# Kernel tuning notes

Measured on AMD Instinct MI355X. Metric: run time of the kernel, lower is better.

The kernel has to match this reference:

```python
import jax, jax.numpy as jnp
import numpy as np

S, B, V, E, H, L = 500, 64, 50257, 512, 512, 2


def setup_inputs() -> dict:
    key = jax.random.key(0)
    ks = jax.random.split(key, 12)
    u = lambda k, shape, s: jax.random.uniform(k, shape, jnp.float32, -s, s)
    kstd = 1.0 / np.sqrt(H)
    return {
        "inputs": jax.random.randint(ks[0], (S, B), 0, V, dtype=jnp.int64),
        "text_lengths": jax.random.randint(ks[1], (B,), 1, S, dtype=jnp.int64),
        "embedding": jax.random.normal(ks[2], (V, E), jnp.float32),
        "W_ih": u(ks[3], (4 * H, E), kstd),   # PyTorch LSTM gate order: i,f,g,o
        "W_hh": u(ks[4], (4 * H, H), kstd),
        "b_ih": u(ks[5], (4 * H,), kstd),
        "b_hh": u(ks[6], (4 * H,), kstd),
        "W_word": u(ks[7], (H, H), 0.1),
        "b_word": jnp.zeros((H, 1), jnp.float32),
        "w_proj": u(ks[8], (H, 1), 0.1),
        "dec_W": u(ks[9], (L, H), kstd),
        "dec_b": u(ks[10], (L,), kstd),
    }


def _lstm(x, W_ih, W_hh, b_ih, b_hh):
    # x: [S, B, E] -> states [S, B, H]
    Bsz = x.shape[1]
    Hn = W_hh.shape[1]
    # precompute input projections for all timesteps in one GEMM
    xproj = jnp.einsum('sbe,ge->sbg', x, W_ih) + b_ih + b_hh  # [S, B, 4H]

    def step(carry, xp):
        h, c = carry
        z = xp + h @ W_hh.T  # [B, 4H]
        i, f, g, o = jnp.split(z, 4, axis=-1)
        i, f, o = jax.nn.sigmoid(i), jax.nn.sigmoid(f), jax.nn.sigmoid(o)
        c = f * c + i * jnp.tanh(g)
        h = o * jnp.tanh(c)
        return (h, c), h

    h0 = jnp.zeros((Bsz, Hn), x.dtype)
    _, hs = jax.lax.scan(step, (h0, h0), xproj)
    return hs  # [S, B, H]


def reference(inputs, text_lengths, embedding, W_ih, W_hh, b_ih, b_hh,
              W_word, b_word, w_proj, dec_W, dec_b):
    # eval mode: dropout is identity
    embedded = embedding[inputs]                       # [S, B, E]
    states = _lstm(embedded, W_ih, W_hh, b_ih, b_hh)   # [S, B, H]
    # batch_matmul_bias with tanh: tanh(states @ W_word + b_word^T)
    word_squish = jnp.tanh(jnp.einsum('sbh,hk->sbk', states, W_word) + b_word[:, 0])
    # batch_matmul: project to scalar score per (s, b)
    word_attn = jnp.einsum('sbh,hk->sbk', word_squish, w_proj)[..., 0]  # [S, B]
    # softmax over sequence dim (nn.Softmax on [B, S] -> dim=1)
    attn = jax.nn.softmax(word_attn.T, axis=1).T       # [S, B]
    # attention_mul: weighted sum over S, keepdim -> [1, B, H]
    pooled = jnp.einsum('sb,sbh->bh', attn, states)[None]
    return pooled @ dec_W.T + dec_b                    # [1, B, labels]
```

## Files before the change

### kernel.cpp

```cpp
#include <hip/hip_runtime.h>


#define S_LEN 500
#define BATCH 64
#define EDIM 512
#define HDIM 512
#define TEAMS 8
#define WGS_PER_TEAM 32
#define TB 8
#define NBLOCKS (TEAMS * WGS_PER_TEAM)
#define NTHREADS 512
#define NSLICE 8
#define SLICE_LEN 63

typedef unsigned long long ull;

#define XPROJ_BYTES  ((size_t)S_LEN * 2048 * BATCH * 4)
#define STATES_OFF   XPROJ_BYTES
#define STATES_BYTES ((size_t)S_LEN * BATCH * HDIM * 4)
#define HBUF_OFF     (STATES_OFF + STATES_BYTES)
#define HBUF_BYTES   ((size_t)2 * TEAMS * TB * HDIM * 8)
#define PART_OFF     (HBUF_OFF + HBUF_BYTES)
#define PART_BYTES   (4 * S_LEN * BATCH * 4)
#define POOLP_OFF    (PART_OFF + PART_BYTES)
#define POOLP_BYTES  ((size_t)BATCH * NSLICE * HDIM * 4)
#define ML_OFF       (POOLP_OFF + POOLP_BYTES)
#define ML_BYTES     (BATCH * NSLICE * 2 * 4)

__global__ __launch_bounds__(256) void xproj_gemm(
    const int* __restrict__ idx, const float* __restrict__ emb,
    const float* __restrict__ W_ih, const float* __restrict__ b_ih,
    const float* __restrict__ b_hh, float* __restrict__ xproj) {
  __shared__ float At[16][132];
  __shared__ float Bt[16][132];
  __shared__ int sidx[128];

  const int tid = threadIdx.x;
  const int sb0 = blockIdx.x * 128;
  const int g0  = blockIdx.y * 128;
  if (tid < 128) sidx[tid] = idx[sb0 + tid];

  const int ty = tid >> 4, tx = tid & 15;
  const int ra = tid & 127, pp = tid >> 7;

  float acc[8][8];
#pragma unroll
  for (int i = 0; i < 8; ++i)
#pragma unroll
    for (int j = 0; j < 8; ++j) acc[i][j] = 0.f;

  __syncthreads();

  for (int k0 = 0; k0 < 512; k0 += 16) {
    const float* pa = &W_ih[(size_t)(g0 + ra) * 512 + k0 + 8 * pp];
    float4 a0 = *(const float4*)pa, a1 = *(const float4*)(pa + 4);
    const float* pb = &emb[(size_t)sidx[ra] * 512 + k0 + 8 * pp];
    float4 b0 = *(const float4*)pb, b1 = *(const float4*)(pb + 4);
    At[8*pp+0][ra]=a0.x; At[8*pp+1][ra]=a0.y; At[8*pp+2][ra]=a0.z; At[8*pp+3][ra]=a0.w;
    At[8*pp+4][ra]=a1.x; At[8*pp+5][ra]=a1.y; At[8*pp+6][ra]=a1.z; At[8*pp+7][ra]=a1.w;
    Bt[8*pp+0][ra]=b0.x; Bt[8*pp+1][ra]=b0.y; Bt[8*pp+2][ra]=b0.z; Bt[8*pp+3][ra]=b0.w;
    Bt[8*pp+4][ra]=b1.x; Bt[8*pp+5][ra]=b1.y; Bt[8*pp+6][ra]=b1.z; Bt[8*pp+7][ra]=b1.w;
    __syncthreads();
#pragma unroll
    for (int kk = 0; kk < 16; ++kk) {
      float4 x0 = *(const float4*)&At[kk][ty * 8];
      float4 x1 = *(const float4*)&At[kk][ty * 8 + 4];
      float4 y0 = *(const float4*)&Bt[kk][tx * 8];
      float4 y1 = *(const float4*)&Bt[kk][tx * 8 + 4];
      float av[8] = {x0.x, x0.y, x0.z, x0.w, x1.x, x1.y, x1.z, x1.w};
      float bv[8] = {y0.x, y0.y, y0.z, y0.w, y1.x, y1.y, y1.z, y1.w};
#pragma unroll
      for (int i = 0; i < 8; ++i)
#pragma unroll
        for (int j = 0; j < 8; ++j) acc[i][j] = fmaf(av[i], bv[j], acc[i][j]);
    }
    __syncthreads();
  }
  const int sbb = sb0 + tx * 8;
  const int s  = sbb >> 6;
  const int tm = (sbb & 63) >> 3;
#pragma unroll
  for (int i = 0; i < 8; ++i) {
    const int g = g0 + ty * 8 + i;
    const float bias = b_ih[g] + b_hh[g];
    float* dst = &xproj[(((size_t)s * TEAMS + tm) * 2048 + g) * 8];
    float4 v0 = {acc[i][0] + bias, acc[i][1] + bias, acc[i][2] + bias, acc[i][3] + bias};
    float4 v1 = {acc[i][4] + bias, acc[i][5] + bias, acc[i][6] + bias, acc[i][7] + bias};
    *(float4*)dst = v0;
    *(float4*)(dst + 4) = v1;
  }
}

__global__ __launch_bounds__(NTHREADS, 1) void lstm_persistent(
    const float* __restrict__ xproj, const float* __restrict__ W_hh,
    float* __restrict__ states, ull* __restrict__ h_buf) {
  __shared__ float red[2][8][4][72];

  const int team = blockIdx.x & 7;
  const int wg   = blockIdx.x >> 3;
  const int tid  = threadIdx.x;
  const int wv   = tid >> 6;
  const int l    = tid & 63;

  const int g = 16 * wg + (l & 15) + 512 * (l >> 4);

  float whh[64];
  {
    const float4* phh = (const float4*)(W_hh + (size_t)g * HDIM + (size_t)wv * 64);
#pragma unroll
    for (int j = 0; j < 16; ++j) {
      float4 v = phh[j];
      whh[4*j+0] = v.x; whh[4*j+1] = v.y; whh[4*j+2] = v.z; whh[4*j+3] = v.w;
    }
  }

  const int gu = l & 15, gbl = l >> 4;
  const int unit = 16 * wg + gu;
  float c_state = 0.f;
  const float* xpbase = xproj + (size_t)(16 * wg + gu) * 8 + (wv * 4 + gbl);

  for (int s = 0; s < S_LEN; ++s) {
    const int par = s & 1, par2 = (s + 1) & 1;

    ull pre0 = 0, pre1 = 0, pre2 = 0, pre3 = 0;
    ull pre4 = 0, pre5 = 0, pre6 = 0, pre7 = 0;
    const ull* hb0 = h_buf + (((size_t)par * TEAMS + team) * TB) * HDIM
                     + (size_t)64 * wv + l;
    if (s > 0) {
      pre0 = __hip_atomic_load(hb0 + 0 * HDIM, __ATOMIC_RELAXED, __HIP_MEMORY_SCOPE_AGENT);
      pre1 = __hip_atomic_load(hb0 + 1 * HDIM, __ATOMIC_RELAXED, __HIP_MEMORY_SCOPE_AGENT);
      pre2 = __hip_atomic_load(hb0 + 2 * HDIM, __ATOMIC_RELAXED, __HIP_MEMORY_SCOPE_AGENT);
      pre3 = __hip_atomic_load(hb0 + 3 * HDIM, __ATOMIC_RELAXED, __HIP_MEMORY_SCOPE_AGENT);
      pre4 = __hip_atomic_load(hb0 + 4 * HDIM, __ATOMIC_RELAXED, __HIP_MEMORY_SCOPE_AGENT);
      pre5 = __hip_atomic_load(hb0 + 5 * HDIM, __ATOMIC_RELAXED, __HIP_MEMORY_SCOPE_AGENT);
      pre6 = __hip_atomic_load(hb0 + 6 * HDIM, __ATOMIC_RELAXED, __HIP_MEMORY_SCOPE_AGENT);
      pre7 = __hip_atomic_load(hb0 + 7 * HDIM, __ATOMIC_RELAXED, __HIP_MEMORY_SCOPE_AGENT);
    }

#pragma unroll
    for (int G = 0; G < 2; ++G) {
      float xv0, xv1, xv2, xv3;
      if (wv == G) {
        const float* p = xpbase + ((size_t)s * TEAMS + team) * (2048 * 8);
        xv0 = p[0]; xv1 = p[512 * 8]; xv2 = p[1024 * 8]; xv3 = p[1536 * 8];
      }

      float acc0 = 0.f, acc1 = 0.f, acc2 = 0.f, acc3 = 0.f;
      if (s > 0) {
        ull r0 = (G == 0) ? pre0 : pre4;
        ull r1 = (G == 0) ? pre1 : pre5;
        ull r2 = (G == 0) ? pre2 : pre6;
        ull r3 = (G == 0) ? pre3 : pre7;
        bool ok = ((int)(r0 >> 32) == s) & ((int)(r1 >> 32) == s) &
                  ((int)(r2 >> 32) == s) & ((int)(r3 >> 32) == s);
        if (!__all(ok)) {
          const ull* hb = hb0 + (size_t)(G * 4) * HDIM;
          int spins = 0;
          for (;;) {
            r0 = __hip_atomic_load(hb + 0 * HDIM, __ATOMIC_RELAXED, __HIP_MEMORY_SCOPE_AGENT);
            r1 = __hip_atomic_load(hb + 1 * HDIM, __ATOMIC_RELAXED, __HIP_MEMORY_SCOPE_AGENT);
            r2 = __hip_atomic_load(hb + 2 * HDIM, __ATOMIC_RELAXED, __HIP_MEMORY_SCOPE_AGENT);
            r3 = __hip_atomic_load(hb + 3 * HDIM, __ATOMIC_RELAXED, __HIP_MEMORY_SCOPE_AGENT);
            ok = ((int)(r0 >> 32) == s) & ((int)(r1 >> 32) == s) &
                 ((int)(r2 >> 32) == s) & ((int)(r3 >> 32) == s);
            if (__all(ok)) break;
            __builtin_amdgcn_s_sleep(1);
            if (++spins > (1 << 18)) break;
          }
        }
        const int h0 = (int)(unsigned)r0, h1 = (int)(unsigned)r1;
        const int h2 = (int)(unsigned)r2, h3 = (int)(unsigned)r3;
#pragma unroll
        for (int k = 0; k < 64; ++k) {
          const float wk = whh[k];
          acc0 = fmaf(wk, __int_as_float(__builtin_amdgcn_readlane(h0, k)), acc0);
          acc1 = fmaf(wk, __int_as_float(__builtin_amdgcn_readlane(h1, k)), acc1);
          acc2 = fmaf(wk, __int_as_float(__builtin_amdgcn_readlane(h2, k)), acc2);
          acc3 = fmaf(wk, __int_as_float(__builtin_amdgcn_readlane(h3, k)), acc3);
        }
      }

      red[G][wv][0][l] = acc0;
      red[G][wv][1][l] = acc1;
      red[G][wv][2][l] = acc2;
      red[G][wv][3][l] = acc3;
      __syncthreads();

      if (wv == G) {
        float z0 = xv0, z1 = xv1, z2 = xv2, z3 = xv3;
#pragma unroll
        for (int w2 = 0; w2 < 8; ++w2) {
          z0 += red[G][w2][gbl][gu +  0];
          z1 += red[G][w2][gbl][gu + 16];
          z2 += red[G][w2][gbl][gu + 32];
          z3 += red[G][w2][gbl][gu + 48];
        }
        float i_ = 1.f / (1.f + expf(-z0));
        float f_ = 1.f / (1.f + expf(-z1));
        float g_ = tanhf(z2);
        float o_ = 1.f / (1.f + expf(-z3));
        c_state = f_ * c_state + i_ * g_;
        float h_ = o_ * tanhf(c_state);
        ull pv = ((ull)(unsigned)(s + 1) << 32) | __float_as_uint(h_);
        __hip_atomic_store(
            &h_buf[(((size_t)par2 * TEAMS + team) * TB + G * 4 + gbl) * HDIM + unit],
            pv, __ATOMIC_RELAXED, __HIP_MEMORY_SCOPE_AGENT);
        states[((size_t)s * BATCH + team * TB + G * 4 + gbl) * HDIM + unit] = h_;
      }
    }
  }
}

#define ATP 132
__global__ __launch_bounds__(256) void attn_gemm(
    const float* __restrict__ states, const float* __restrict__ W_word,
    const float* __restrict__ b_word, const float* __restrict__ w_proj,
    float* __restrict__ part) {
  __shared__ float At[16][ATP];
  __shared__ float Bt[16][ATP];
  __shared__ float redl[128][17];

  const int tid = threadIdx.x;
  const int m0 = blockIdx.x * 128;
  const int n0 = blockIdx.y * 128;
  const int ty = tid >> 4, tx = tid & 15;

  float acc[8][8];
#pragma unroll
  for (int i = 0; i < 8; ++i)
#pragma unroll
    for (int j = 0; j < 8; ++j) acc[i][j] = 0.f;

  for (int k0 = 0; k0 < 512; k0 += 16) {
#pragma unroll
    for (int it = 0; it < 2; ++it) {
      int m = (tid >> 2) + 64 * it;
      int kq = tid & 3;
      float4 v = *(const float4*)&states[(size_t)(m0 + m) * 512 + k0 + 4 * kq];
      At[4 * kq + 0][m] = v.x; At[4 * kq + 1][m] = v.y;
      At[4 * kq + 2][m] = v.z; At[4 * kq + 3][m] = v.w;
    }
#pragma unroll
    for (int it = 0; it < 2; ++it) {
      int kr = (tid >> 5) + 8 * it;
      int nq = tid & 31;
      float4 v = *(const float4*)&W_word[(size_t)(k0 + kr) * 512 + n0 + 4 * nq];
      *(float4*)&Bt[kr][4 * nq] = v;
    }
    __syncthreads();
#pragma unroll
    for (int kk = 0; kk < 16; ++kk) {
      float4 a0 = *(const float4*)&At[kk][ty * 8];
      float4 a1 = *(const float4*)&At[kk][ty * 8 + 4];
      float4 b0 = *(const float4*)&Bt[kk][tx * 8];
      float4 b1 = *(const float4*)&Bt[kk][tx * 8 + 4];
      float av[8] = {a0.x, a0.y, a0.z, a0.w, a1.x, a1.y, a1.z, a1.w};
      float bv[8] = {b0.x, b0.y, b0.z, b0.w, b1.x, b1.y, b1.z, b1.w};
#pragma unroll
      for (int i = 0; i < 8; ++i)
#pragma unroll
        for (int j = 0; j < 8; ++j) acc[i][j] = fmaf(av[i], bv[j], acc[i][j]);
    }
    __syncthreads();
  }
  float bw[8], wp[8];
  {
    float4 v0 = *(const float4*)&b_word[n0 + tx * 8];
    float4 v1 = *(const float4*)&b_word[n0 + tx * 8 + 4];
    bw[0]=v0.x; bw[1]=v0.y; bw[2]=v0.z; bw[3]=v0.w; bw[4]=v1.x; bw[5]=v1.y; bw[6]=v1.z; bw[7]=v1.w;
    float4 u0 = *(const float4*)&w_proj[n0 + tx * 8];
    float4 u1 = *(const float4*)&w_proj[n0 + tx * 8 + 4];
    wp[0]=u0.x; wp[1]=u0.y; wp[2]=u0.z; wp[3]=u0.w; wp[4]=u1.x; wp[5]=u1.y; wp[6]=u1.z; wp[7]=u1.w;
  }
#pragma unroll
  for (int i = 0; i < 8; ++i) {
    float rs = 0.f;
#pragma unroll
    for (int j = 0; j < 8; ++j) rs += tanhf(acc[i][j] + bw[j]) * wp[j];
    redl[ty * 8 + i][tx] = rs;
  }
  __syncthreads();
  if (tid < 128) {
    float ssum = 0.f;
#pragma unroll
    for (int x = 0; x < 16; ++x) ssum += redl[tid][x];
    part[(size_t)blockIdx.y * (S_LEN * BATCH) + m0 + tid] = ssum;
  }
}

__global__ __launch_bounds__(256) void pool_partial(
    const float* __restrict__ part, const float* __restrict__ states,
    float* __restrict__ poolP, float* __restrict__ ml) {
  const int b = blockIdx.x >> 3;
  const int sl = blockIdx.x & 7;
  const int s0 = sl * SLICE_LEN;
  const int len = (sl == 7) ? (S_LEN - 7 * SLICE_LEN) : SLICE_LEN;
  const int tid = threadIdx.x;

  __shared__ float es[SLICE_LEN];
  __shared__ float redm[256];

  float sc = -1e30f;
  if (tid < len) {
    const int t = (s0 + tid) * BATCH + b;
    sc = part[t] + part[S_LEN * BATCH + t] + part[2 * S_LEN * BATCH + t] +
         part[3 * S_LEN * BATCH + t];
  }
  redm[tid] = sc;
  __syncthreads();
  for (int o = 128; o > 0; o >>= 1) {
    if (tid < o) redm[tid] = fmaxf(redm[tid], redm[tid + o]);
    __syncthreads();
  }
  const float m_sl = redm[0];
  __syncthreads();
  float e = 0.f;
  if (tid < len) e = expf(sc - m_sl);
  if (tid < SLICE_LEN) es[tid] = (tid < len) ? e : 0.f;
  redm[tid] = e;
  __syncthreads();
  for (int o = 128; o > 0; o >>= 1) {
    if (tid < o) redm[tid] += redm[tid + o];
    __syncthreads();
  }
  if (tid == 0) {
    ml[(b * NSLICE + sl) * 2 + 0] = m_sl;
    ml[(b * NSLICE + sl) * 2 + 1] = redm[0];
  }
  __syncthreads();

  for (int h = tid; h < HDIM; h += 256) {
    float a = 0.f;
    for (int s = 0; s < len; ++s)
      a = fmaf(es[s], states[((size_t)(s0 + s) * BATCH + b) * HDIM + h], a);
    poolP[((size_t)b * NSLICE + sl) * HDIM + h] = a;
  }
}

__global__ __launch_bounds__(256) void pool_merge_decode(
    const float* __restrict__ poolP, const float* __restrict__ ml,
    const float* __restrict__ dec_W, const float* __restrict__ dec_b,
    float* __restrict__ out) {
  const int b = blockIdx.x;
  const int tid = threadIdx.x;
  __shared__ float pool[HDIM];
  __shared__ float redm[256];
  __shared__ float wsl[NSLICE];

  if (tid == 0) {
    float gmax = -1e30f;
#pragma unroll
    for (int i = 0; i < NSLICE; ++i) gmax = fmaxf(gmax, ml[(b * NSLICE + i) * 2]);
    float Z = 0.f;
#pragma unroll
    for (int i = 0; i < NSLICE; ++i) {
      float w = expf(ml[(b * NSLICE + i) * 2] - gmax);
      wsl[i] = w;
      Z = fmaf(ml[(b * NSLICE + i) * 2 + 1], w, Z);
    }
    redm[0] = 1.f / Z;
  }
  __syncthreads();
  const float inv = redm[0];

  for (int h = tid; h < HDIM; h += 256) {
    float a = 0.f;
#pragma unroll
    for (int i = 0; i < NSLICE; ++i)
      a = fmaf(wsl[i], poolP[((size_t)b * NSLICE + i) * HDIM + h], a);
    pool[h] = a * inv;
  }
  __syncthreads();
  const int lcls = tid >> 7, ch = tid & 127;
  float p = 0.f;
#pragma unroll
  for (int j = 0; j < 4; ++j)
    p = fmaf(pool[ch * 4 + j], dec_W[lcls * HDIM + ch * 4 + j], p);
  redm[tid] = p;
  __syncthreads();
  for (int o = 64; o > 0; o >>= 1) {
    if (ch < o) redm[tid] += redm[tid + o];
    __syncthreads();
  }
  if (ch == 0) out[b * 2 + lcls] = redm[tid] + dec_b[lcls];
}

extern "C" void kernel_launch(void* const* d_in, const int* in_sizes, int n_in,
                              void* d_out, int out_size, void* d_ws, size_t ws_size,
                              hipStream_t stream) {
  const int*   idx    = (const int*)d_in[0];
  const float* emb    = (const float*)d_in[2];
  const float* W_ih   = (const float*)d_in[3];
  const float* W_hh   = (const float*)d_in[4];
  const float* b_ih   = (const float*)d_in[5];
  const float* b_hh   = (const float*)d_in[6];
  const float* W_word = (const float*)d_in[7];
  const float* b_word = (const float*)d_in[8];
  const float* w_proj = (const float*)d_in[9];
  const float* dec_W  = (const float*)d_in[10];
  const float* dec_b  = (const float*)d_in[11];
  float* out = (float*)d_out;

  char* ws = (char*)d_ws;
  float* xproj  = (float*)ws;
  float* states = (float*)(ws + STATES_OFF);
  ull*   h_buf  = (ull*)(ws + HBUF_OFF);
  float* part   = (float*)(ws + PART_OFF);
  float* poolP  = (float*)(ws + POOLP_OFF);
  float* ml     = (float*)(ws + ML_OFF);

  hipMemsetAsync(h_buf, 0, HBUF_BYTES, stream);

  xproj_gemm<<<dim3(250, 16), 256, 0, stream>>>(idx, emb, W_ih, b_ih, b_hh, xproj);

  void* args[] = {(void*)&xproj, (void*)&W_hh, (void*)&states, (void*)&h_buf};
  hipLaunchCooperativeKernel(lstm_persistent, dim3(NBLOCKS), dim3(NTHREADS), args, 0, stream);

  attn_gemm<<<dim3(250, 4), 256, 0, stream>>>(states, W_word, b_word, w_proj, part);
  pool_partial<<<BATCH * NSLICE, 256, 0, stream>>>(part, states, poolP, ml);
  pool_merge_decode<<<BATCH, 256, 0, stream>>>(poolP, ml, dec_W, dec_b, out);
}
```

Measured before the change: 3.113 ms.

## Use split-bf16 MFMA for LSTM recurrent matvec instead of readlane FMAs

Replaces the per-lane scalar FMA loop with readlane broadcasts in the persistent LSTM kernel with MFMA 16x16x32 bf16 instructions. W_hh and h are each split into hi and lo bf16 parts, and three MFMAs per tile approximate fp32 accuracy. The h polling is restructured so only the 4 active batch columns load 16 values each, and the reduction shared-memory layout is changed to match the MFMA output. It wastes 12 of the 16 MFMA columns, since only 4 batch rows are active, and adds conversion work each step. It also drops the early prefetch of h_buf before the gate loop.

```diff
diff --git a/kernel.cpp b/kernel.cpp
--- a/kernel.cpp
+++ b/kernel.cpp
@@ -14,6 +14,9 @@
 #define SLICE_LEN 63
 
 typedef unsigned long long ull;
+typedef __attribute__((ext_vector_type(8))) short short8v;
+typedef __attribute__((ext_vector_type(4))) float float4v;
+typedef __attribute__((ext_vector_type(4))) unsigned int uint4v;
 
 #define XPROJ_BYTES  ((size_t)S_LEN * 2048 * BATCH * 4)
 #define STATES_OFF   XPROJ_BYTES
@@ -94,7 +97,7 @@
 __global__ __launch_bounds__(NTHREADS, 1) void lstm_persistent(
     const float* __restrict__ xproj, const float* __restrict__ W_hh,
     float* __restrict__ states, ull* __restrict__ h_buf) {
-  __shared__ float red[2][8][4][72];
+  __shared__ float red[2][8][4][16][5];
 
   const int team = blockIdx.x & 7;
   const int wg   = blockIdx.x >> 3;
@@ -102,40 +105,41 @@
   const int wv   = tid >> 6;
   const int l    = tid & 63;
 
-  const int g = 16 * wg + (l & 15) + 512 * (l >> 4);
-
-  float whh[64];
-  {
-    const float4* phh = (const float4*)(W_hh + (size_t)g * HDIM + (size_t)wv * 64);
-#pragma unroll
-    for (int j = 0; j < 16; ++j) {
-      float4 v = phh[j];
-      whh[4*j+0] = v.x; whh[4*j+1] = v.y; whh[4*j+2] = v.z; whh[4*j+3] = v.w;
-    }
-  }
+  const int col = l & 15;
+  const int kg  = l >> 4;
+
+  short8v Ahi[4][2], Alo[4][2];
+#pragma unroll
+  for (int j = 0; j < 4; ++j)
+#pragma unroll
+    for (int ks = 0; ks < 2; ++ks) {
+      const float* wr = &W_hh[((size_t)(16 * wg + col) + 512 * j) * 512
+                              + 64 * wv + 32 * ks + 8 * kg];
+      unsigned hw[4], lw[4];
+#pragma unroll
+      for (int p = 0; p < 4; ++p) {
+        float w0 = wr[2 * p], w1 = wr[2 * p + 1];
+        unsigned u0 = __float_as_uint(w0), u1 = __float_as_uint(w1);
+        hw[p] = (u1 & 0xffff0000u) | (u0 >> 16);
+        float l0 = w0 - __uint_as_float(u0 & 0xffff0000u);
+        float l1 = w1 - __uint_as_float(u1 & 0xffff0000u);
+        lw[p] = (__float_as_uint(l1) & 0xffff0000u) | (__float_as_uint(l0) >> 16);
+      }
+      uint4v ph = {hw[0], hw[1], hw[2], hw[3]};
+      uint4v pl = {lw[0], lw[1], lw[2], lw[3]};
+      Ahi[j][ks] = __builtin_bit_cast(short8v, ph);
+      Alo[j][ks] = __builtin_bit_cast(short8v, pl);
+    }
 
   const int gu = l & 15, gbl = l >> 4;
   const int unit = 16 * wg + gu;
   float c_state = 0.f;
   const float* xpbase = xproj + (size_t)(16 * wg + gu) * 8 + (wv * 4 + gbl);
 
+  const bool bact = (col < 4);
+
   for (int s = 0; s < S_LEN; ++s) {
     const int par = s & 1, par2 = (s + 1) & 1;
-
-    ull pre0 = 0, pre1 = 0, pre2 = 0, pre3 = 0;
-    ull pre4 = 0, pre5 = 0, pre6 = 0, pre7 = 0;
-    const ull* hb0 = h_buf + (((size_t)par * TEAMS + team) * TB) * HDIM
-                     + (size_t)64 * wv + l;
-    if (s > 0) {
-      pre0 = __hip_atomic_load(hb0 + 0 * HDIM, __ATOMIC_RELAXED, __HIP_MEMORY_SCOPE_AGENT);
-      pre1 = __hip_atomic_load(hb0 + 1 * HDIM, __ATOMIC_RELAXED, __HIP_MEMORY_SCOPE_AGENT);
-      pre2 = __hip_atomic_load(hb0 + 2 * HDIM, __ATOMIC_RELAXED, __HIP_MEMORY_SCOPE_AGENT);
-      pre3 = __hip_atomic_load(hb0 + 3 * HDIM, __ATOMIC_RELAXED, __HIP_MEMORY_SCOPE_AGENT);
-      pre4 = __hip_atomic_load(hb0 + 4 * HDIM, __ATOMIC_RELAXED, __HIP_MEMORY_SCOPE_AGENT);
-      pre5 = __hip_atomic_load(hb0 + 5 * HDIM, __ATOMIC_RELAXED, __HIP_MEMORY_SCOPE_AGENT);
-      pre6 = __hip_atomic_load(hb0 + 6 * HDIM, __ATOMIC_RELAXED, __HIP_MEMORY_SCOPE_AGENT);
-      pre7 = __hip_atomic_load(hb0 + 7 * HDIM, __ATOMIC_RELAXED, __HIP_MEMORY_SCOPE_AGENT);
-    }
 
 #pragma unroll
     for (int G = 0; G < 2; ++G) {
@@ -145,55 +149,82 @@
         xv0 = p[0]; xv1 = p[512 * 8]; xv2 = p[1024 * 8]; xv3 = p[1536 * 8];
       }
 
-      float acc0 = 0.f, acc1 = 0.f, acc2 = 0.f, acc3 = 0.f;
+      float4v acc[4];
+#pragma unroll
+      for (int j = 0; j < 4; ++j) acc[j] = (float4v){0.f, 0.f, 0.f, 0.f};
+
       if (s > 0) {
-        ull r0 = (G == 0) ? pre0 : pre4;
-        ull r1 = (G == 0) ? pre1 : pre5;
-        ull r2 = (G == 0) ? pre2 : pre6;
-        ull r3 = (G == 0) ? pre3 : pre7;
-        bool ok = ((int)(r0 >> 32) == s) & ((int)(r1 >> 32) == s) &
-                  ((int)(r2 >> 32) == s) & ((int)(r3 >> 32) == s);
-        if (!__all(ok)) {
-          const ull* hb = hb0 + (size_t)(G * 4) * HDIM;
-          int spins = 0;
-          for (;;) {
-            r0 = __hip_atomic_load(hb + 0 * HDIM, __ATOMIC_RELAXED, __HIP_MEMORY_SCOPE_AGENT);
-            r1 = __hip_atomic_load(hb + 1 * HDIM, __ATOMIC_RELAXED, __HIP_MEMORY_SCOPE_AGENT);
-            r2 = __hip_atomic_load(hb + 2 * HDIM, __ATOMIC_RELAXED, __HIP_MEMORY_SCOPE_AGENT);
-            r3 = __hip_atomic_load(hb + 3 * HDIM, __ATOMIC_RELAXED, __HIP_MEMORY_SCOPE_AGENT);
-            ok = ((int)(r0 >> 32) == s) & ((int)(r1 >> 32) == s) &
-                 ((int)(r2 >> 32) == s) & ((int)(r3 >> 32) == s);
-            if (__all(ok)) break;
-            __builtin_amdgcn_s_sleep(1);
-            if (++spins > (1 << 18)) break;
+        const int bcol = bact ? col : 0;
+        const ull* hbb = h_buf + (((size_t)par * TEAMS + team) * TB + G * 4 + bcol) * HDIM
+                         + (size_t)64 * wv + 8 * kg;
+        ull rr[16];
+#pragma unroll
+        for (int q = 0; q < 16; ++q) rr[q] = 0;
+        int spins = 0;
+        for (;;) {
+          bool ok = true;
+          if (bact) {
+#pragma unroll
+            for (int ks = 0; ks < 2; ++ks)
+#pragma unroll
+              for (int i = 0; i < 8; ++i)
+                rr[ks * 8 + i] = __hip_atomic_load(hbb + 32 * ks + i,
+                                                   __ATOMIC_RELAXED,
+                                                   __HIP_MEMORY_SCOPE_AGENT);
+#pragma unroll
+            for (int q = 0; q < 16; ++q) ok &= ((int)(rr[q] >> 32) == s);
+          }
+          if (__all(ok)) break;
+          __builtin_amdgcn_s_sleep(1);
+          if (++spins > (1 << 18)) break;
+        }
+        short8v Bhi[2], Blo[2];
+#pragma unroll
+        for (int ks = 0; ks < 2; ++ks) {
+          unsigned hw[4], lw[4];
+#pragma unroll
+          for (int p = 0; p < 4; ++p) {
+            float f0 = bact ? __uint_as_float((unsigned)rr[ks * 8 + 2 * p]) : 0.f;
+            float f1 = bact ? __uint_as_float((unsigned)rr[ks * 8 + 2 * p + 1]) : 0.f;
+            unsigned u0 = __float_as_uint(f0), u1 = __float_as_uint(f1);
+            hw[p] = (u1 & 0xffff0000u) | (u0 >> 16);
+            float l0 = f0 - __uint_as_float(u0 & 0xffff0000u);
+            float l1 = f1 - __uint_as_float(u1 & 0xffff0000u);
+            lw[p] = (__float_as_uint(l1) & 0xffff0000u) | (__float_as_uint(l0) >> 16);
+          }
+          uint4v ph = {hw[0], hw[1], hw[2], hw[3]};
+          uint4v pl = {lw[0], lw[1], lw[2], lw[3]};
+          Bhi[ks] = __builtin_bit_cast(short8v, ph);
+          Blo[ks] = __builtin_bit_cast(short8v, pl);
+        }
+#pragma unroll
+        for (int j = 0; j < 4; ++j) {
+#pragma unroll
+          for (int ks = 0; ks < 2; ++ks) {
+            acc[j] = __builtin_amdgcn_mfma_f32_16x16x32_bf16(Ahi[j][ks], Bhi[ks], acc[j], 0, 0, 0);
+            acc[j] = __builtin_amdgcn_mfma_f32_16x16x32_bf16(Alo[j][ks], Bhi[ks], acc[j], 0, 0, 0);
+            acc[j] = __builtin_amdgcn_mfma_f32_16x16x32_bf16(Ahi[j][ks], Blo[ks], acc[j], 0, 0, 0);
           }
         }
-        const int h0 = (int)(unsigned)r0, h1 = (int)(unsigned)r1;
-        const int h2 = (int)(unsigned)r2, h3 = (int)(unsigned)r3;
-#pragma unroll
-        for (int k = 0; k < 64; ++k) {
-          const float wk = whh[k];
-          acc0 = fmaf(wk, __int_as_float(__builtin_amdgcn_readlane(h0, k)), acc0);
-          acc1 = fmaf(wk, __int_as_float(__builtin_amdgcn_readlane(h1, k)), acc1);
-          acc2 = fmaf(wk, __int_as_float(__builtin_amdgcn_readlane(h2, k)), acc2);
-          acc3 = fmaf(wk, __int_as_float(__builtin_amdgcn_readlane(h3, k)), acc3);
-        }
       }
 
-      red[G][wv][0][l] = acc0;
-      red[G][wv][1][l] = acc1;
-      red[G][wv][2][l] = acc2;
-      red[G][wv][3][l] = acc3;
+      if (bact) {
+#pragma unroll
+        for (int j = 0; j < 4; ++j)
+#pragma unroll
+          for (int r = 0; r < 4; ++r)
+            red[G][wv][j][kg * 4 + r][col] = acc[j][r];
+      }
       __syncthreads();
 
       if (wv == G) {
         float z0 = xv0, z1 = xv1, z2 = xv2, z3 = xv3;
 #pragma unroll
         for (int w2 = 0; w2 < 8; ++w2) {
-          z0 += red[G][w2][gbl][gu +  0];
-          z1 += red[G][w2][gbl][gu + 16];
-          z2 += red[G][w2][gbl][gu + 32];
-          z3 += red[G][w2][gbl][gu + 48];
+          z0 += red[G][w2][0][gu][gbl];
+          z1 += red[G][w2][1][gu][gbl];
+          z2 += red[G][w2][2][gu][gbl];
+          z3 += red[G][w2][3][gu][gbl];
         }
         float i_ = 1.f / (1.f + expf(-z0));
         float f_ = 1.f / (1.f + expf(-z1));
```

After: 3.507 ms. +12.6%, slower.
